# Kernel optimization log

Hardware: AMD Instinct MI355X
Metric: run time of the kernel (lower is better)

## Reference

```python
import jax, jax.numpy as jnp
import numpy as np

S, XD, C, R = 6, 3, 8, 64   # num_freqs, x_dim, num_channels, res_scale
N = 262144
STD = 0.001


def setup_inputs() -> dict:
    key = jax.random.key(0)
    k1, k2, k3 = jax.random.split(key, 3)
    x = jax.random.uniform(k1, (N, XD), dtype=jnp.float32)
    features = jax.random.normal(k2, (S, 2 * XD, C, R, R), dtype=jnp.float32) * STD
    features_2d = jax.random.normal(k3, (S, 2 * XD, C, R, R), dtype=jnp.float32) * STD
    return {"x": x, "features": features, "features_2d": features_2d}


def _bilinear(img, gx, gy):
    # img: [C,H,W]; gx,gy: [P] normalized coords in [-1,1]
    # bilinear grid_sample, align_corners=True, clamped (border) indices
    _, H, W = img.shape
    ix = (gx + 1.0) * 0.5 * (W - 1)
    iy = (gy + 1.0) * 0.5 * (H - 1)
    ix0f = jnp.floor(ix)
    iy0f = jnp.floor(iy)
    wx = ix - ix0f
    wy = iy - iy0f
    ix0 = jnp.clip(ix0f.astype(jnp.int32), 0, W - 1)
    iy0 = jnp.clip(iy0f.astype(jnp.int32), 0, H - 1)
    ix1 = jnp.clip(ix0 + 1, 0, W - 1)
    iy1 = jnp.clip(iy0 + 1, 0, H - 1)
    v00 = img[:, iy0, ix0]  # [C,P]
    v01 = img[:, iy0, ix1]
    v10 = img[:, iy1, ix0]
    v11 = img[:, iy1, ix1]
    return (v00 * (1 - wx) * (1 - wy) + v01 * wx * (1 - wy)
            + v10 * (1 - wx) * wy + v11 * wx * wy)


def reference(x, features, features_2d):
    n = x.shape[0]
    scales = 2.0 ** jnp.arange(S, dtype=x.dtype)                   # [S]
    xb = x[:, None, :] * scales[:, None]                           # [N,S,3]
    latent = jnp.sin(jnp.stack([xb, xb + 0.5 * jnp.pi], axis=-2))  # [N,S,2,3]

    B = S * 2 * XD  # 36 independent (scale, sin/cos, dim) lookups

    # 1D (line) lookup: grid x-coord fixed at 0, y-coord = encoded value
    gy = jnp.transpose(latent.reshape(n, S, 2 * XD), (1, 2, 0)).reshape(B, n)
    gx = jnp.zeros_like(gy)
    fs = jax.vmap(_bilinear)(features.reshape(B, C, R, R), gx, gy)  # [B,C,N]
    fs = fs.reshape(S, 2, XD, C, n)

    # 2D (plane) lookup with cyclic dim pairs (1,2),(2,0),(0,1)
    pairs = jnp.array([[1, 2], [2, 0], [0, 1]])
    g2 = latent[..., pairs]                                        # [N,S,2,3,2]
    gx2 = jnp.transpose(g2[..., 0], (1, 2, 3, 0)).reshape(B, n)
    gy2 = jnp.transpose(g2[..., 1], (1, 2, 3, 0)).reshape(B, n)
    fs2 = jax.vmap(_bilinear)(features_2d.reshape(B, C, R, R), gx2, gy2)
    fs2 = fs2.reshape(S, 2, XD, C, n)

    out = jnp.transpose(fs * fs2, (4, 3, 0, 1, 2))                 # [N,C,S,2,3]
    out = out + latent[:, None]                                    # + PE, broadcast over C
    return out.reshape(n, C * S * 2 * XD)                          # [N, 288]
```

## Files before the change

kernel.cpp:

```cpp
#include <hip/hip_runtime.h>

#define NS 6
#define NXD 3
#define NC 8
#define NR 64
#define NB 36
#define NPOINTS 262144
#define OUTD 288
#define PTS 32

__device__ __forceinline__ unsigned short f2bf(float f) {
    unsigned u = __float_as_uint(f);
    unsigned r = u + 0x7fffu + ((u >> 16) & 1u);
    return (unsigned short)(r >> 16);
}
__device__ __forceinline__ unsigned pack2(float a, float b) {
    return (unsigned)f2bf(a) | ((unsigned)f2bf(b) << 16);
}

__global__ void build_px(const float* __restrict__ F2, unsigned* __restrict__ px) {
    int tid = blockIdx.x * 256 + threadIdx.x;
    const int total = NB * 65 * 64 * NC;
    if (tid >= total) return;
    int c = tid & 7;
    int xx = (tid >> 3) & 63;
    int rest = tid >> 9;
    int y = rest % 65;
    int b = rest / 65;
    int ys = y < 63 ? y : 63;
    const float* src = F2 + (((size_t)(b * NC + c) * NR + ys) * NR);
    float v0 = src[xx];
    float v1 = src[xx < 63 ? xx + 1 : 63];
    px[tid] = pack2(v0, v1);
}

__global__ void build_f1q(const float* __restrict__ F, unsigned* __restrict__ f1q) {
    int tid = blockIdx.x * 256 + threadIdx.x;
    const int total = NB * 64 * NC;
    if (tid >= total) return;
    int c = tid & 7;
    int y = (tid >> 3) & 63;
    int b = tid >> 9;
    const float* img = F + (size_t)(b * NC + c) * NR * NR;
    float a = 0.5f * (img[y * NR + 31] + img[y * NR + 32]);
    int y1 = y < 63 ? y + 1 : 63;
    float bb = 0.5f * (img[y1 * NR + 31] + img[y1 * NR + 32]);
    f1q[tid] = pack2(a, bb);
}

__global__ __launch_bounds__(256, 3) void encode_kernel(
    const float* __restrict__ x,
    const unsigned* __restrict__ px,
    const unsigned* __restrict__ f1q,
    float* __restrict__ out)
{
    __shared__ float lat[PTS][NB];
    __shared__ float stage[PTS * 289];
    const int t = threadIdx.x;
    const int c = t & 7;
    const int u = t >> 3;
    const int n = blockIdx.x * PTS + u;

    const float xv0 = x[3 * n + 0];
    const float xv1 = x[3 * n + 1];
    const float xv2 = x[3 * n + 2];

    #pragma unroll
    for (int ii = 0; ii < 5; ++ii) {
        int i = c + ii * 8;
        if (i < NB) {
            int s = i / 6;
            int rr = i - s * 6;
            int p = rr / 3;
            int d = rr - p * 3;
            float xb = (d == 0 ? xv0 : (d == 1 ? xv1 : xv2)) * (float)(1 << s);
            lat[u][i] = p ? __cosf(xb) : __sinf(xb);
        }
    }
    __syncthreads();

    const float* latu = lat[u];
    float* stg = &stage[u * 289];

    for (int g = 0; g < 12; ++g) {
        const int b0 = g * 3;
        #pragma unroll
        for (int k = 0; k < 3; ++k) {
            const int b = b0 + k;
            const int i0 = b0 + (k == 0 ? 1 : (k == 1 ? 2 : 0));
            const int i1 = b0 + (k == 0 ? 2 : (k == 1 ? 0 : 1));
            float gy1 = latu[b];
            float ga = latu[i0];
            float gb = latu[i1];

            float fy = fminf(fmaxf(__builtin_fmaf(gy1, 31.5f, 31.5f), 0.0f), 63.0f);
            float fy0 = floorf(fy);
            float wy = fy - fy0;
            int y0 = (int)fy0;
            unsigned pr = f1q[(b * 64 + y0) * 8 + c];
            float a0 = __uint_as_float(pr << 16);
            float a1 = __uint_as_float(pr & 0xffff0000u);
            float fsv = __builtin_fmaf(a1 - a0, wy, a0);

            float fx2 = fminf(fmaxf(__builtin_fmaf(ga, 31.5f, 31.5f), 0.0f), 63.0f);
            float fy2 = fminf(fmaxf(__builtin_fmaf(gb, 31.5f, 31.5f), 0.0f), 63.0f);
            float fx20 = floorf(fx2);
            float fy20 = floorf(fy2);
            float wx2 = fx2 - fx20;
            float wy2 = fy2 - fy20;
            int xx = (int)fx20;
            int yy = (int)fy20;
            const unsigned* rb = px + ((b * 65 + yy) * 64 + xx) * 8 + c;
            unsigned top = rb[0];
            unsigned bot = rb[512];
            float v00 = __uint_as_float(top << 16);
            float v01 = __uint_as_float(top & 0xffff0000u);
            float v10 = __uint_as_float(bot << 16);
            float v11 = __uint_as_float(bot & 0xffff0000u);
            float tp = __builtin_fmaf(v01 - v00, wx2, v00);
            float bt = __builtin_fmaf(v11 - v10, wx2, v10);
            float fs2v = __builtin_fmaf(bt - tp, wy2, tp);

            stg[c * 36 + b] = __builtin_fmaf(fsv, fs2v, gy1);
        }
    }
    __syncthreads();

    float* ob = out + (size_t)blockIdx.x * (PTS * OUTD);
    #pragma unroll
    for (int r = 0; r < 36; ++r) {
        int e = t + r * 256;
        int uu = e / 288;
        int v = e - uu * 288;
        ob[e] = stage[uu * 289 + v];
    }
}

extern "C" void kernel_launch(void* const* d_in, const int* in_sizes, int n_in,
                              void* d_out, int out_size, void* d_ws, size_t ws_size,
                              hipStream_t stream)
{
    const float* x  = (const float*)d_in[0];
    const float* F  = (const float*)d_in[1];
    const float* F2 = (const float*)d_in[2];
    float* out = (float*)d_out;

    unsigned* px  = (unsigned*)d_ws;
    unsigned* f1q = px + NB * 65 * 64 * NC;

    build_px<<<(NB * 65 * 64 * NC + 255) / 256, 256, 0, stream>>>(F2, px);
    build_f1q<<<(NB * 64 * NC + 255) / 256, 256, 0, stream>>>(F, f1q);
    encode_kernel<<<NPOINTS / PTS, 256, 0, stream>>>(x, px, f1q, out);
}
```

Before: 399.7 us.

## Pack 2x2 bilinear texels into uint2 and compute sin/cos per thread

The plane table now stores both bilinear rows (top and bottom bf16 pairs) in one uint2 entry, so each 2D lookup is a single 8-byte gather instead of two 4-byte loads 512 entries apart. The shared-memory latent table and its barrier are dropped: each thread recomputes the sin/cos values itself per scale group, which adds redundant transcendental work across the 8 channel threads. The occupancy hint rises from 3 to 4 blocks per SM. The plane table doubles in size, so it occupies more cache.

```diff
diff --git a/kernel.cpp b/kernel.cpp
--- a/kernel.cpp
+++ b/kernel.cpp
@@ -18,20 +18,20 @@
     return (unsigned)f2bf(a) | ((unsigned)f2bf(b) << 16);
 }
 
-__global__ void build_px(const float* __restrict__ F2, unsigned* __restrict__ px) {
+__global__ void build_px2(const float* __restrict__ F2, uint2* __restrict__ px) {
     int tid = blockIdx.x * 256 + threadIdx.x;
-    const int total = NB * 65 * 64 * NC;
+    const int total = NB * 64 * 64 * NC;
     if (tid >= total) return;
-    int c = tid & 7;
+    int c  = tid & 7;
     int xx = (tid >> 3) & 63;
-    int rest = tid >> 9;
-    int y = rest % 65;
-    int b = rest / 65;
-    int ys = y < 63 ? y : 63;
-    const float* src = F2 + (((size_t)(b * NC + c) * NR + ys) * NR);
-    float v0 = src[xx];
-    float v1 = src[xx < 63 ? xx + 1 : 63];
-    px[tid] = pack2(v0, v1);
+    int y  = (tid >> 9) & 63;
+    int b  = tid >> 15;
+    const float* img = F2 + (size_t)(b * NC + c) * (NR * NR);
+    int x1 = xx < 63 ? xx + 1 : 63;
+    int y1 = y  < 63 ? y  + 1 : 63;
+    unsigned top = pack2(img[y  * NR + xx], img[y  * NR + x1]);
+    unsigned bot = pack2(img[y1 * NR + xx], img[y1 * NR + x1]);
+    px[tid] = make_uint2(top, bot);
 }
 
 __global__ void build_f1q(const float* __restrict__ F, unsigned* __restrict__ f1q) {
@@ -48,13 +48,12 @@
     f1q[tid] = pack2(a, bb);
 }
 
-__global__ __launch_bounds__(256, 3) void encode_kernel(
+__global__ __launch_bounds__(256, 4) void encode_kernel(
     const float* __restrict__ x,
-    const unsigned* __restrict__ px,
+    const uint2* __restrict__ px,
     const unsigned* __restrict__ f1q,
     float* __restrict__ out)
 {
-    __shared__ float lat[PTS][NB];
     __shared__ float stage[PTS * 289];
     const int t = threadIdx.x;
     const int c = t & 7;
@@ -65,33 +64,26 @@
     const float xv1 = x[3 * n + 1];
     const float xv2 = x[3 * n + 2];
 
-    #pragma unroll
-    for (int ii = 0; ii < 5; ++ii) {
-        int i = c + ii * 8;
-        if (i < NB) {
-            int s = i / 6;
-            int rr = i - s * 6;
-            int p = rr / 3;
-            int d = rr - p * 3;
-            float xb = (d == 0 ? xv0 : (d == 1 ? xv1 : xv2)) * (float)(1 << s);
-            lat[u][i] = p ? __cosf(xb) : __sinf(xb);
-        }
-    }
-    __syncthreads();
-
-    const float* latu = lat[u];
     float* stg = &stage[u * 289];
 
+    #pragma unroll
     for (int g = 0; g < 12; ++g) {
+        const int s = g >> 1;
+        const int p = g & 1;
+        const float sc = (float)(1 << s);
+        float l0, l1, l2;
+        if (p == 0) {
+            l0 = __sinf(xv0 * sc); l1 = __sinf(xv1 * sc); l2 = __sinf(xv2 * sc);
+        } else {
+            l0 = __cosf(xv0 * sc); l1 = __cosf(xv1 * sc); l2 = __cosf(xv2 * sc);
+        }
         const int b0 = g * 3;
         #pragma unroll
         for (int k = 0; k < 3; ++k) {
             const int b = b0 + k;
-            const int i0 = b0 + (k == 0 ? 1 : (k == 1 ? 2 : 0));
-            const int i1 = b0 + (k == 0 ? 2 : (k == 1 ? 0 : 1));
-            float gy1 = latu[b];
-            float ga = latu[i0];
-            float gb = latu[i1];
+            float gy1 = (k == 0) ? l0 : (k == 1) ? l1 : l2;
+            float ga  = (k == 0) ? l1 : (k == 1) ? l2 : l0;
+            float gb  = (k == 0) ? l2 : (k == 1) ? l0 : l1;
 
             float fy = fminf(fmaxf(__builtin_fmaf(gy1, 31.5f, 31.5f), 0.0f), 63.0f);
             float fy0 = floorf(fy);
@@ -110,13 +102,11 @@
             float wy2 = fy2 - fy20;
             int xx = (int)fx20;
             int yy = (int)fy20;
-            const unsigned* rb = px + ((b * 65 + yy) * 64 + xx) * 8 + c;
-            unsigned top = rb[0];
-            unsigned bot = rb[512];
-            float v00 = __uint_as_float(top << 16);
-            float v01 = __uint_as_float(top & 0xffff0000u);
-            float v10 = __uint_as_float(bot << 16);
-            float v11 = __uint_as_float(bot & 0xffff0000u);
+            uint2 pp = px[((b * 64 + yy) * 64 + xx) * 8 + c];
+            float v00 = __uint_as_float(pp.x << 16);
+            float v01 = __uint_as_float(pp.x & 0xffff0000u);
+            float v10 = __uint_as_float(pp.y << 16);
+            float v11 = __uint_as_float(pp.y & 0xffff0000u);
             float tp = __builtin_fmaf(v01 - v00, wx2, v00);
             float bt = __builtin_fmaf(v11 - v10, wx2, v10);
             float fs2v = __builtin_fmaf(bt - tp, wy2, tp);
@@ -145,10 +135,10 @@
     const float* F2 = (const float*)d_in[2];
     float* out = (float*)d_out;
 
-    unsigned* px  = (unsigned*)d_ws;
-    unsigned* f1q = px + NB * 65 * 64 * NC;
+    uint2* px     = (uint2*)d_ws;
+    unsigned* f1q = (unsigned*)((char*)d_ws + (size_t)NB * 64 * 64 * NC * 8);
 
-    build_px<<<(NB * 65 * 64 * NC + 255) / 256, 256, 0, stream>>>(F2, px);
+    build_px2<<<(NB * 64 * 64 * NC + 255) / 256, 256, 0, stream>>>(F2, px);
     build_f1q<<<(NB * 64 * NC + 255) / 256, 256, 0, stream>>>(F, f1q);
     encode_kernel<<<NPOINTS / PTS, 256, 0, stream>>>(x, px, f1q, out);
 }
```

Result: faster. 381.3 us (-4.6%).
